# Kernel optimization log

Measured on AMD Instinct MI355X. Metric: run time of the kernel, lower is better.

Reference implementation:

```python
import jax, jax.numpy as jnp
import numpy as np

N_NODES = 100000
N_EDGES = 3200000
N_GRAPHS = 64


def _gcn_conv(x, W, b, row, col, norm, n):
    # GCNConv: linear transform, then normalized scatter-add aggregation, then bias
    h = x @ W                                  # [N, H]
    msg = h[row] * norm[:, None]               # gather + scale, [E+N, H]
    out = jax.ops.segment_sum(msg, col, num_segments=n)
    return out + b


def setup_inputs() -> dict:
    key = jax.random.key(0)
    ks = jax.random.split(key, 8)
    x = jax.random.normal(ks[0], (N_NODES, 128), dtype=jnp.float32)
    edge_index = jax.random.randint(ks[1], (2, N_EDGES), 0, N_NODES, dtype=jnp.int64)
    batch = jnp.sort(jax.random.randint(ks[2], (N_NODES,), 0, N_GRAPHS, dtype=jnp.int64))
    W1 = jax.random.normal(ks[3], (128, 256), dtype=jnp.float32) * (1.0 / np.sqrt(128))
    b1 = jnp.zeros((256,), dtype=jnp.float32)
    W2 = jax.random.normal(ks[4], (256, 256), dtype=jnp.float32) * (1.0 / np.sqrt(256))
    b2 = jnp.zeros((256,), dtype=jnp.float32)
    Wl = jax.random.normal(ks[5], (256, 2), dtype=jnp.float32) * (1.0 / np.sqrt(256))
    bl = jnp.zeros((2,), dtype=jnp.float32)
    return {"x": x, "edge_index": edge_index, "batch": batch,
            "W1": W1, "b1": b1, "W2": W2, "b2": b2, "Wl": Wl, "bl": bl}


def reference(x, edge_index, batch, W1, b1, W2, b2, Wl, bl):
    n = x.shape[0]
    # add self-loops (PyG GCNConv default)
    loop = jnp.arange(n, dtype=edge_index.dtype)
    row = jnp.concatenate([edge_index[0], loop])   # source
    col = jnp.concatenate([edge_index[1], loop])   # target
    # symmetric normalization: deg computed on targets (with self-loops)
    deg = jax.ops.segment_sum(jnp.ones_like(col, dtype=x.dtype), col, num_segments=n)
    dinv = jnp.where(deg > 0, jax.lax.rsqrt(deg), 0.0)
    norm = dinv[row] * dinv[col]

    h = jax.nn.relu(_gcn_conv(x, W1, b1, row, col, norm, n))
    # dropout p=0.1 is identity at inference (training=False)
    h = jax.nn.relu(_gcn_conv(h, W2, b2, row, col, norm, n))

    # global mean pool over graphs
    sums = jax.ops.segment_sum(h, batch, num_segments=N_GRAPHS)
    cnts = jax.ops.segment_sum(jnp.ones((n,), dtype=h.dtype), batch, num_segments=N_GRAPHS)
    pooled = sums / jnp.maximum(cnts, 1.0)[:, None]

    return pooled @ Wl + bl
```

## Files before the change

kernel.cpp:

```cpp
#include <hip/hip_runtime.h>
#include <hip/hip_bf16.h>
#include <cstddef>

#define NODES  100000
#define EDGES  3200000
#define ETOT   3300000
#define NGRAPH 64
#define HDIM   256
#define BSHIFT 9
#define NBUCK  196
#define BCAP   19456

typedef __hip_bfloat16 bf16;
typedef short bf16x8 __attribute__((ext_vector_type(8)));
typedef float f32x4 __attribute__((ext_vector_type(4)));
typedef float f32x2 __attribute__((ext_vector_type(2)));
typedef unsigned u32x2 __attribute__((ext_vector_type(2)));
typedef unsigned u32x4 __attribute__((ext_vector_type(4)));

__global__ void xcast_kernel(const float* __restrict__ x, const float* __restrict__ dinv,
                             unsigned char* __restrict__ x8) {
    int i = blockIdx.x * 256 + threadIdx.x;
    if ((size_t)i * 4 >= (size_t)NODES * 128) return;
    float d = dinv[i >> 5];
    float4 v = *(const float4*)(x + (size_t)i * 4);
    int w = __builtin_amdgcn_cvt_pk_fp8_f32(v.x * d, v.y * d, 0, false);
    w     = __builtin_amdgcn_cvt_pk_fp8_f32(v.z * d, v.w * d, w, true);
    *(unsigned*)(x8 + (size_t)i * 4) = (unsigned)w;
}

__global__ void wcast_kernel(const float* __restrict__ W1, const float* __restrict__ W2,
                             bf16* __restrict__ W1t, bf16* __restrict__ W2t) {
    int i = blockIdx.x * 256 + threadIdx.x;
    if (i < 128 * 256) {
        int n = i / 128, k = i - n * 128;
        W1t[i] = __float2bfloat16(W1[(size_t)k * 256 + n]);
    } else if (i < 128 * 256 + 256 * 256) {
        int q = i - 128 * 256;
        int n = q / 256, k = q - n * 256;
        W2t[q] = __float2bfloat16(W2[(size_t)k * 256 + n]);
    }
}

__global__ __launch_bounds__(1024) void fillp1_kernel(const int* __restrict__ row,
                                                      const int* __restrict__ col,
                                                      int* __restrict__ gcnt,
                                                      unsigned* __restrict__ recs) {
    __shared__ int hist[4][NBUCK];
    __shared__ int coff[4][NBUCK];
    __shared__ int base[NBUCK];
    int t  = threadIdx.x;
    int cp = t & 3;
    for (int i = t; i < 4 * NBUCK; i += 1024) ((int*)hist)[i] = 0;
    __syncthreads();
    int e0 = blockIdx.x * 16384;
    int r[16], c[16], rk[16];
    #pragma unroll
    for (int i = 0; i < 16; i++) {
        int e = e0 + i * 1024 + t;
        r[i] = -1;
        if (e < ETOT) {
            if (e < EDGES) { r[i] = row[e]; c[i] = col[e]; }
            else           { r[i] = e - EDGES; c[i] = r[i]; }
            rk[i] = atomicAdd(&hist[cp][c[i] >> BSHIFT], 1);
        }
    }
    __syncthreads();
    if (t < NBUCK) {
        int h0 = hist[0][t], h1 = hist[1][t], h2 = hist[2][t], h3 = hist[3][t];
        coff[0][t] = 0; coff[1][t] = h0; coff[2][t] = h0 + h1; coff[3][t] = h0 + h1 + h2;
        int tot = h0 + h1 + h2 + h3;
        base[t] = (tot > 0) ? atomicAdd(&gcnt[t], tot) : 0;
    }
    __syncthreads();
    #pragma unroll
    for (int i = 0; i < 16; i++) {
        if (r[i] >= 0) {
            int b = c[i] >> BSHIFT;
            recs[(size_t)b * BCAP + base[b] + coff[cp][b] + rk[i]] =
                ((unsigned)r[i] << BSHIFT) | (unsigned)(c[i] & 511);
        }
    }
}

__global__ void bscan_kernel(const int* __restrict__ gcnt, int* __restrict__ bbase) {
    __shared__ int part[256];
    int t = threadIdx.x;
    int v0 = (t < NBUCK) ? gcnt[t] : 0;
    part[t] = v0;
    __syncthreads();
    for (int off = 1; off < 256; off <<= 1) {
        int v = (t >= off) ? part[t - off] : 0;
        __syncthreads();
        part[t] += v;
        __syncthreads();
    }
    if (t < NBUCK) bbase[t] = part[t] - v0;
}

__global__ __launch_bounds__(256) void build_kernel(const unsigned* __restrict__ recs,
                                                    const int* __restrict__ gcnt,
                                                    const int* __restrict__ bbase,
                                                    int* __restrict__ rowptr,
                                                    float* __restrict__ dinv,
                                                    int* __restrict__ csr) {
    __shared__ int hist[512];
    __shared__ int cur[512];
    __shared__ int part[256];
    const int b = blockIdx.x, t = threadIdx.x;
    const int cnt = gcnt[b];
    const int base = bbase[b];
    const int n0 = b << BSHIFT;
    hist[t] = 0; hist[t + 256] = 0;
    __syncthreads();
    const unsigned* rb = recs + (size_t)b * BCAP;
    for (int i = t; i < cnt; i += 256) atomicAdd(&hist[rb[i] & 511u], 1);
    __syncthreads();
    int h0 = hist[2 * t], h1 = hist[2 * t + 1];
    part[t] = h0 + h1;
    __syncthreads();
    for (int off = 1; off < 256; off <<= 1) {
        int v = (t >= off) ? part[t - off] : 0;
        __syncthreads();
        part[t] += v;
        __syncthreads();
    }
    int ex = (t == 0) ? 0 : part[t - 1];
    cur[2 * t]     = ex;
    cur[2 * t + 1] = ex + h0;
    int v0 = n0 + 2 * t, v1 = v0 + 1;
    if (v0 < NODES) { rowptr[v0] = base + ex;      dinv[v0] = rsqrtf((float)h0); }
    if (v1 < NODES) { rowptr[v1] = base + ex + h0; dinv[v1] = rsqrtf((float)h1); }
    if (b == 0 && t == 0) rowptr[NODES] = ETOT;
    __syncthreads();
    for (int i = t; i < cnt; i += 256) {
        unsigned r = rb[i];
        int pos = atomicAdd(&cur[r & 511u], 1);
        csr[base + pos] = (int)(r >> BSHIFT);
    }
}

__global__ void agg1_kernel(const unsigned char* __restrict__ x8, const int* __restrict__ rowptr,
                            const int* __restrict__ csr, const float* __restrict__ dinv,
                            bf16* __restrict__ out) {
    int w    = (blockIdx.x * blockDim.x + threadIdx.x) >> 6;
    int lane = threadIdx.x & 63;
    int half = lane >> 5, li = lane & 31;
    int node = w * 2 + half;
    if (node >= NODES) return;
    int beg = rowptr[node], end = rowptr[node + 1];
    float a0 = 0.f, a1 = 0.f, a2 = 0.f, a3 = 0.f;
    int j = beg;
#define ACC4(q) do {                                                       \
        f32x2 d0 = __builtin_amdgcn_cvt_pk_f32_fp8((int)(q), false);       \
        f32x2 d1 = __builtin_amdgcn_cvt_pk_f32_fp8((int)(q), true);        \
        a0 += d0.x; a1 += d0.y; a2 += d1.x; a3 += d1.y;                    \
    } while (0)
    for (; j + 3 < end; j += 4) {
        int s0 = csr[j], s1 = csr[j + 1], s2 = csr[j + 2], s3 = csr[j + 3];
        unsigned q0 = *(const unsigned*)(x8 + (size_t)s0 * 128 + li * 4);
        unsigned q1 = *(const unsigned*)(x8 + (size_t)s1 * 128 + li * 4);
        unsigned q2 = *(const unsigned*)(x8 + (size_t)s2 * 128 + li * 4);
        unsigned q3 = *(const unsigned*)(x8 + (size_t)s3 * 128 + li * 4);
        ACC4(q0); ACC4(q1); ACC4(q2); ACC4(q3);
    }
    for (; j < end; j++) {
        unsigned q0 = *(const unsigned*)(x8 + (size_t)csr[j] * 128 + li * 4);
        ACC4(q0);
    }
#undef ACC4
    float d = dinv[node];
    union { __hip_bfloat162 h[2]; u32x2 u; } pk;
    pk.h[0] = __float22bfloat162_rn(make_float2(a0 * d, a1 * d));
    pk.h[1] = __float22bfloat162_rn(make_float2(a2 * d, a3 * d));
    *(u32x2*)(out + (size_t)node * 128 + li * 4) = pk.u;
}

__global__ void agg2_kernel(const unsigned char* __restrict__ h8, const int* __restrict__ rowptr,
                            const int* __restrict__ csr, const float* __restrict__ dinv,
                            bf16* __restrict__ out) {
    int w    = (blockIdx.x * blockDim.x + threadIdx.x) >> 6;
    int lane = threadIdx.x & 63;
    int half = lane >> 5, li = lane & 31;
    int node = w * 2 + half;
    if (node >= NODES) return;
    int beg = rowptr[node], end = rowptr[node + 1];
    float a[8] = {};
    int j = beg;
#define ACC8(q) do {                                                       \
        f32x2 d0 = __builtin_amdgcn_cvt_pk_f32_fp8((int)(q).x, false);     \
        f32x2 d1 = __builtin_amdgcn_cvt_pk_f32_fp8((int)(q).x, true);      \
        f32x2 d2 = __builtin_amdgcn_cvt_pk_f32_fp8((int)(q).y, false);     \
        f32x2 d3 = __builtin_amdgcn_cvt_pk_f32_fp8((int)(q).y, true);      \
        a[0] += d0.x; a[1] += d0.y; a[2] += d1.x; a[3] += d1.y;            \
        a[4] += d2.x; a[5] += d2.y; a[6] += d3.x; a[7] += d3.y;            \
    } while (0)
    for (; j + 3 < end; j += 4) {
        int s0 = csr[j], s1 = csr[j + 1], s2 = csr[j + 2], s3 = csr[j + 3];
        u32x2 q0 = *(const u32x2*)(h8 + (size_t)s0 * 256 + li * 8);
        u32x2 q1 = *(const u32x2*)(h8 + (size_t)s1 * 256 + li * 8);
        u32x2 q2 = *(const u32x2*)(h8 + (size_t)s2 * 256 + li * 8);
        u32x2 q3 = *(const u32x2*)(h8 + (size_t)s3 * 256 + li * 8);
        ACC8(q0); ACC8(q1); ACC8(q2); ACC8(q3);
    }
    for (; j < end; j++) {
        u32x2 q0 = *(const u32x2*)(h8 + (size_t)csr[j] * 256 + li * 8);
        ACC8(q0);
    }
#undef ACC8
    float d = dinv[node];
    union { __hip_bfloat162 h[4]; u32x4 u; } pk;
    pk.h[0] = __float22bfloat162_rn(make_float2(a[0] * d, a[1] * d));
    pk.h[1] = __float22bfloat162_rn(make_float2(a[2] * d, a[3] * d));
    pk.h[2] = __float22bfloat162_rn(make_float2(a[4] * d, a[5] * d));
    pk.h[3] = __float22bfloat162_rn(make_float2(a[6] * d, a[7] * d));
    *(u32x4*)(out + (size_t)node * 256 + li * 8) = pk.u;
}

template <int K, bool PRESCALE>
__global__ __launch_bounds__(256) void mgemm_kernel(const bf16* __restrict__ A,
                                                    const bf16* __restrict__ Bt,
                                                    const float* __restrict__ bias,
                                                    const float* __restrict__ dinv,
                                                    unsigned char* __restrict__ C8) {
    __shared__ short As[128][40];
    __shared__ short Bs[128][40];
    const int t    = threadIdx.x;
    const int bm   = (int)(blockIdx.x >> 1) * 128;
    const int bn   = (int)(blockIdx.x & 1) * 128;
    const int lane = t & 63;
    const int wave = t >> 6;
    const int wm   = (wave >> 1) * 64, wn = (wave & 1) * 64;
    const int m16  = lane & 15, kq = lane >> 4;
    f32x4 acc[4][4] = {};

    for (int k0 = 0; k0 < K; k0 += 32) {
        #pragma unroll
        for (int h = 0; h < 2; h++) {
            int q = t * 2 + h;
            int rr = q >> 2, seg = q & 3;
            uint4 va = {0u, 0u, 0u, 0u};
            int grow = bm + rr;
            if (grow < NODES) va = *(const uint4*)(A + (size_t)grow * K + k0 + seg * 8);
            *(uint4*)&As[rr][seg * 8] = va;
            uint4 vb = *(const uint4*)(Bt + (size_t)(bn + rr) * K + k0 + seg * 8);
            *(uint4*)&Bs[rr][seg * 8] = vb;
        }
        __syncthreads();
        bf16x8 af[4], bf_[4];
        #pragma unroll
        for (int i = 0; i < 4; i++) {
            af[i]  = *(const bf16x8*)&As[wm + i * 16 + m16][kq * 8];
            bf_[i] = *(const bf16x8*)&Bs[wn + i * 16 + m16][kq * 8];
        }
        #pragma unroll
        for (int mt = 0; mt < 4; mt++)
            #pragma unroll
            for (int nt = 0; nt < 4; nt++)
                acc[mt][nt] = __builtin_amdgcn_mfma_f32_16x16x32_bf16(af[mt], bf_[nt],
                                                                     acc[mt][nt], 0, 0, 0);
        __syncthreads();
    }

    #pragma unroll
    for (int mt = 0; mt < 4; mt++) {
        #pragma unroll
        for (int r = 0; r < 4; r++) {
            int row = bm + wm + mt * 16 + kq * 4 + r;
            if (row >= NODES) continue;
            float sc = PRESCALE ? dinv[row] : 1.f;
            #pragma unroll
            for (int nt = 0; nt < 4; nt++) {
                int colb = bn + wn + nt * 16 + m16;
                float v = fmaxf(acc[mt][nt][r] + bias[colb], 0.f) * sc;
                int pkd = __builtin_amdgcn_cvt_pk_fp8_f32(v, v, 0, false);
                C8[(size_t)row * 256 + colb] = (unsigned char)(pkd & 0xff);
            }
        }
    }
}

__global__ void pool_kernel(const unsigned char* __restrict__ h2, const int* __restrict__ batch,
                            float* __restrict__ sums) {
    int lane = threadIdx.x & 63;
    int sub  = threadIdx.x >> 6;
    int r0   = blockIdx.x * 1024 + sub * 256;
    if (r0 >= NODES) return;
    int r1 = r0 + 256; if (r1 > NODES) r1 = NODES;
    float a0 = 0.f, a1 = 0.f, a2 = 0.f, a3 = 0.f;
    int g = batch[r0];
    int cb = lane * 4;
    for (int r = r0; r < r1; r++) {
        int gg = batch[r];
        if (gg != g) {
            atomicAdd(&sums[g * 256 + cb + 0], a0);
            atomicAdd(&sums[g * 256 + cb + 1], a1);
            atomicAdd(&sums[g * 256 + cb + 2], a2);
            atomicAdd(&sums[g * 256 + cb + 3], a3);
            a0 = a1 = a2 = a3 = 0.f; g = gg;
        }
        unsigned q = *(const unsigned*)(h2 + (size_t)r * 256 + cb);
        f32x2 d0 = __builtin_amdgcn_cvt_pk_f32_fp8((int)q, false);
        f32x2 d1 = __builtin_amdgcn_cvt_pk_f32_fp8((int)q, true);
        a0 += d0.x; a1 += d0.y; a2 += d1.x; a3 += d1.y;
    }
    atomicAdd(&sums[g * 256 + cb + 0], a0);
    atomicAdd(&sums[g * 256 + cb + 1], a1);
    atomicAdd(&sums[g * 256 + cb + 2], a2);
    atomicAdd(&sums[g * 256 + cb + 3], a3);
}

__global__ void final_kernel(const float* __restrict__ sums, const int* __restrict__ batch,
                             const float* __restrict__ Wl, const float* __restrict__ bl,
                             float* __restrict__ out) {
    int g = blockIdx.x;
    int l = threadIdx.x;
    int lo = 0, hi = NODES;
    while (lo < hi) { int m = (lo + hi) >> 1; if (batch[m] < g) lo = m + 1; else hi = m; }
    int lb = lo;
    lo = lb; hi = NODES;
    while (lo < hi) { int m = (lo + hi) >> 1; if (batch[m] <= g) lo = m + 1; else hi = m; }
    int cnt = lo - lb;
    float inv = 1.f / fmaxf((float)cnt, 1.f);
    float a0 = 0.f, a1 = 0.f;
    for (int k = l; k < 256; k += 64) {
        float p = sums[g * 256 + k] * inv;
        a0 += p * Wl[k * 2 + 0];
        a1 += p * Wl[k * 2 + 1];
    }
    for (int off = 32; off > 0; off >>= 1) {
        a0 += __shfl_down(a0, off, 64);
        a1 += __shfl_down(a1, off, 64);
    }
    if (l == 0) {
        out[g * 2 + 0] = a0 + bl[0];
        out[g * 2 + 1] = a1 + bl[1];
    }
}

extern "C" void kernel_launch(void* const* d_in, const int* in_sizes, int n_in,
                              void* d_out, int out_size, void* d_ws, size_t ws_size,
                              hipStream_t stream) {
    const float* x    = (const float*)d_in[0];
    const int*   ei   = (const int*)d_in[1];
    const int*   bat  = (const int*)d_in[2];
    const float* W1   = (const float*)d_in[3];
    const float* b1   = (const float*)d_in[4];
    const float* W2   = (const float*)d_in[5];
    const float* b2   = (const float*)d_in[6];
    const float* Wl   = (const float*)d_in[7];
    const float* bl   = (const float*)d_in[8];
    float*       out  = (float*)d_out;
    const int* erow = ei;
    const int* ecol = ei + EDGES;

    char* p = (char*)d_ws;
    auto take = [&](size_t bytes) {
        char* r = p;
        p += (bytes + 255) & ~(size_t)255;
        return r;
    };
    float* dinv   = (float*)take((size_t)NODES * 4);
    int*   rowptr = (int*)  take((size_t)(NODES + 1) * 4);
    int*   gcnt   = (int*)  take((size_t)NBUCK * 4);
    int*   bbase  = (int*)  take((size_t)NBUCK * 4);
    int*   csr    = (int*)  take((size_t)ETOT * 4);
    float* sums   = (float*)take((size_t)NGRAPH * HDIM * 4);
    bf16*  W1t    = (bf16*) take((size_t)128 * 256 * 2);
    bf16*  W2t    = (bf16*) take((size_t)256 * 256 * 2);
    char*  reg1   = (char*) take((size_t)NODES * HDIM * 1);
    char*  reg2   = (char*) take((size_t)NODES * HDIM * 2);
    char*  reg3   = (char*) take((size_t)NODES * HDIM * 1);
    unsigned char* x8      = (unsigned char*)reg1;
    unsigned char* h1f8    = (unsigned char*)reg1;
    bf16*          aggbuf1 = (bf16*)reg2;
    bf16*          aggbuf2 = (bf16*)reg2;
    unsigned*      recs    = (unsigned*)reg3;
    unsigned char* h2f8    = (unsigned char*)reg3;

    hipMemsetAsync(sums, 0, (size_t)NGRAPH * HDIM * 4, stream);
    hipMemsetAsync(gcnt, 0, (size_t)NBUCK * 4, stream);
    wcast_kernel<<<(128 * 256 + 256 * 256 + 255) / 256, 256, 0, stream>>>(W1, W2, W1t, W2t);

    fillp1_kernel<<<(ETOT + 16383) / 16384, 1024, 0, stream>>>(erow, ecol, gcnt, recs);
    bscan_kernel <<<1, 256, 0, stream>>>(gcnt, bbase);
    build_kernel <<<NBUCK, 256, 0, stream>>>(recs, gcnt, bbase, rowptr, dinv, csr);

    xcast_kernel<<<(NODES * 128 / 4 + 255) / 256, 256, 0, stream>>>(x, dinv, x8);

    const int AGG_BLOCKS = (NODES / 2 * 64) / 256;
    agg1_kernel<<<AGG_BLOCKS, 256, 0, stream>>>(x8, rowptr, csr, dinv, aggbuf1);

    const int MB = (NODES + 127) / 128;
    mgemm_kernel<128, true ><<<MB * 2, 256, 0, stream>>>(aggbuf1, W1t, b1, dinv, h1f8);

    agg2_kernel<<<AGG_BLOCKS, 256, 0, stream>>>(h1f8, rowptr, csr, dinv, aggbuf2);

    mgemm_kernel<256, false><<<MB * 2, 256, 0, stream>>>(aggbuf2, W2t, b2, nullptr, h2f8);

    pool_kernel<<<(NODES + 1023) / 1024, 256, 0, stream>>>(h2f8, bat, sums);

    final_kernel<<<NGRAPH, 64, 0, stream>>>(sums, bat, Wl, bl, out);
}
```

Measured before the change: 555.8 us.

## Store aggregation outputs as fp8 and fold bucket scan into build kernel

The aggregation kernels now write their normalized sums as packed fp8 instead of bf16, and the GEMM loads fp8 A tiles and expands them to bf16 in shared memory. This halves the intermediate buffer traffic between the aggregation and GEMM stages, at the cost of extra conversion work in the GEMM load path and lower precision of the GEMM input. Separately, the single-block bucket prefix-scan kernel is removed: each build block now reduces the counts of preceding buckets itself, which saves one launch but adds redundant work per block.

```diff
diff --git a/kernel.cpp b/kernel.cpp
--- a/kernel.cpp
+++ b/kernel.cpp
@@ -83,34 +83,27 @@
     }
 }
 
-__global__ void bscan_kernel(const int* __restrict__ gcnt, int* __restrict__ bbase) {
-    __shared__ int part[256];
-    int t = threadIdx.x;
-    int v0 = (t < NBUCK) ? gcnt[t] : 0;
-    part[t] = v0;
-    __syncthreads();
-    for (int off = 1; off < 256; off <<= 1) {
-        int v = (t >= off) ? part[t - off] : 0;
-        __syncthreads();
-        part[t] += v;
-        __syncthreads();
-    }
-    if (t < NBUCK) bbase[t] = part[t] - v0;
-}
-
 __global__ __launch_bounds__(256) void build_kernel(const unsigned* __restrict__ recs,
                                                     const int* __restrict__ gcnt,
-                                                    const int* __restrict__ bbase,
                                                     int* __restrict__ rowptr,
                                                     float* __restrict__ dinv,
                                                     int* __restrict__ csr) {
     __shared__ int hist[512];
     __shared__ int cur[512];
     __shared__ int part[256];
+    __shared__ int sbase;
     const int b = blockIdx.x, t = threadIdx.x;
     const int cnt = gcnt[b];
-    const int base = bbase[b];
     const int n0 = b << BSHIFT;
+    part[t] = (t < b) ? gcnt[t] : 0;
+    __syncthreads();
+    for (int off = 128; off >= 1; off >>= 1) {
+        if (t < off) part[t] += part[t + off];
+        __syncthreads();
+    }
+    if (t == 0) sbase = part[0];
+    __syncthreads();
+    const int base = sbase;
     hist[t] = 0; hist[t + 256] = 0;
     __syncthreads();
     const unsigned* rb = recs + (size_t)b * BCAP;
@@ -142,7 +135,7 @@
 
 __global__ void agg1_kernel(const unsigned char* __restrict__ x8, const int* __restrict__ rowptr,
                             const int* __restrict__ csr, const float* __restrict__ dinv,
-                            bf16* __restrict__ out) {
+                            unsigned char* __restrict__ out) {
     int w    = (blockIdx.x * blockDim.x + threadIdx.x) >> 6;
     int lane = threadIdx.x & 63;
     int half = lane >> 5, li = lane & 31;
@@ -170,15 +163,14 @@
     }
 #undef ACC4
     float d = dinv[node];
-    union { __hip_bfloat162 h[2]; u32x2 u; } pk;
-    pk.h[0] = __float22bfloat162_rn(make_float2(a0 * d, a1 * d));
-    pk.h[1] = __float22bfloat162_rn(make_float2(a2 * d, a3 * d));
-    *(u32x2*)(out + (size_t)node * 128 + li * 4) = pk.u;
+    int pk = __builtin_amdgcn_cvt_pk_fp8_f32(a0 * d, a1 * d, 0, false);
+    pk     = __builtin_amdgcn_cvt_pk_fp8_f32(a2 * d, a3 * d, pk, true);
+    *(unsigned*)(out + (size_t)node * 128 + li * 4) = (unsigned)pk;
 }
 
 __global__ void agg2_kernel(const unsigned char* __restrict__ h8, const int* __restrict__ rowptr,
                             const int* __restrict__ csr, const float* __restrict__ dinv,
-                            bf16* __restrict__ out) {
+                            unsigned char* __restrict__ out) {
     int w    = (blockIdx.x * blockDim.x + threadIdx.x) >> 6;
     int lane = threadIdx.x & 63;
     int half = lane >> 5, li = lane & 31;
@@ -209,16 +201,17 @@
     }
 #undef ACC8
     float d = dinv[node];
-    union { __hip_bfloat162 h[4]; u32x4 u; } pk;
-    pk.h[0] = __float22bfloat162_rn(make_float2(a[0] * d, a[1] * d));
-    pk.h[1] = __float22bfloat162_rn(make_float2(a[2] * d, a[3] * d));
-    pk.h[2] = __float22bfloat162_rn(make_float2(a[4] * d, a[5] * d));
-    pk.h[3] = __float22bfloat162_rn(make_float2(a[6] * d, a[7] * d));
-    *(u32x4*)(out + (size_t)node * 256 + li * 8) = pk.u;
+    u32x2 o;
+    int p0 = __builtin_amdgcn_cvt_pk_fp8_f32(a[0] * d, a[1] * d, 0, false);
+    p0     = __builtin_amdgcn_cvt_pk_fp8_f32(a[2] * d, a[3] * d, p0, true);
+    int p1 = __builtin_amdgcn_cvt_pk_fp8_f32(a[4] * d, a[5] * d, 0, false);
+    p1     = __builtin_amdgcn_cvt_pk_fp8_f32(a[6] * d, a[7] * d, p1, true);
+    o.x = (unsigned)p0; o.y = (unsigned)p1;
+    *(u32x2*)(out + (size_t)node * 256 + li * 8) = o;
 }
 
 template <int K, bool PRESCALE>
-__global__ __launch_bounds__(256) void mgemm_kernel(const bf16* __restrict__ A,
+__global__ __launch_bounds__(256) void mgemm_kernel(const unsigned char* __restrict__ A8,
                                                     const bf16* __restrict__ Bt,
                                                     const float* __restrict__ bias,
                                                     const float* __restrict__ dinv,
@@ -235,14 +228,26 @@
     f32x4 acc[4][4] = {};
 
     for (int k0 = 0; k0 < K; k0 += 32) {
+        {
+            int rr = t >> 1, seg = t & 1;
+            uint4 va = {0u, 0u, 0u, 0u};
+            int grow = bm + rr;
+            if (grow < NODES) va = *(const uint4*)(A8 + (size_t)grow * K + k0 + seg * 16);
+            unsigned wd[4] = {va.x, va.y, va.z, va.w};
+            #pragma unroll
+            for (int u = 0; u < 4; u++) {
+                f32x2 lo = __builtin_amdgcn_cvt_pk_f32_fp8((int)wd[u], false);
+                f32x2 hi = __builtin_amdgcn_cvt_pk_f32_fp8((int)wd[u], true);
+                union { __hip_bfloat162 h[2]; u32x2 q; } pk;
+                pk.h[0] = __float22bfloat162_rn(make_float2(lo.x, lo.y));
+                pk.h[1] = __float22bfloat162_rn(make_float2(hi.x, hi.y));
+                *(u32x2*)&As[rr][seg * 16 + u * 4] = pk.q;
+            }
+        }
         #pragma unroll
         for (int h = 0; h < 2; h++) {
             int q = t * 2 + h;
             int rr = q >> 2, seg = q & 3;
-            uint4 va = {0u, 0u, 0u, 0u};
-            int grow = bm + rr;
-            if (grow < NODES) va = *(const uint4*)(A + (size_t)grow * K + k0 + seg * 8);
-            *(uint4*)&As[rr][seg * 8] = va;
             uint4 vb = *(const uint4*)(Bt + (size_t)(bn + rr) * K + k0 + seg * 8);
             *(uint4*)&Bs[rr][seg * 8] = vb;
         }
@@ -363,18 +368,17 @@
     float* dinv   = (float*)take((size_t)NODES * 4);
     int*   rowptr = (int*)  take((size_t)(NODES + 1) * 4);
     int*   gcnt   = (int*)  take((size_t)NBUCK * 4);
-    int*   bbase  = (int*)  take((size_t)NBUCK * 4);
     int*   csr    = (int*)  take((size_t)ETOT * 4);
     float* sums   = (float*)take((size_t)NGRAPH * HDIM * 4);
     bf16*  W1t    = (bf16*) take((size_t)128 * 256 * 2);
     bf16*  W2t    = (bf16*) take((size_t)256 * 256 * 2);
     char*  reg1   = (char*) take((size_t)NODES * HDIM * 1);
-    char*  reg2   = (char*) take((size_t)NODES * HDIM * 2);
+    char*  reg2   = (char*) take((size_t)NODES * HDIM * 1);
     char*  reg3   = (char*) take((size_t)NODES * HDIM * 1);
     unsigned char* x8      = (unsigned char*)reg1;
     unsigned char* h1f8    = (unsigned char*)reg1;
-    bf16*          aggbuf1 = (bf16*)reg2;
-    bf16*          aggbuf2 = (bf16*)reg2;
+    unsigned char* aggbuf1 = (unsigned char*)reg2;
+    unsigned char* aggbuf2 = (unsigned char*)reg2;
     unsigned*      recs    = (unsigned*)reg3;
     unsigned char* h2f8    = (unsigned char*)reg3;
 
@@ -383,8 +387,7 @@
     wcast_kernel<<<(128 * 256 + 256 * 256 + 255) / 256, 256, 0, stream>>>(W1, W2, W1t, W2t);
 
     fillp1_kernel<<<(ETOT + 16383) / 16384, 1024, 0, stream>>>(erow, ecol, gcnt, recs);
-    bscan_kernel <<<1, 256, 0, stream>>>(gcnt, bbase);
-    build_kernel <<<NBUCK, 256, 0, stream>>>(recs, gcnt, bbase, rowptr, dinv, csr);
+    build_kernel <<<NBUCK, 256, 0, stream>>>(recs, gcnt, rowptr, dinv, csr);
 
     xcast_kernel<<<(NODES * 128 / 4 + 255) / 256, 256, 0, stream>>>(x, dinv, x8);
 
```

Result: faster. 535.4 us, median of 2 (-3.7%).
